# Optimization experiments

Measured on AMD Instinct MI355X. Metric: run time of the kernel, lower is better.

## Reference

```python
import jax, jax.numpy as jnp
import numpy as np

B = 32768          # batch size (positions)
PIECES = 32        # max active features per position
NNZ = B * PIECES
FT_OUT = 512
NFEAT = 768        # 64 squares * 6 piece types * 2 colors


def setup_inputs() -> dict:
    key = jax.random.key(0)
    k1, k2, k3, k4, k5, k6 = jax.random.split(key, 6)
    rows = jnp.repeat(jnp.arange(B, dtype=jnp.int64), PIECES)  # batch index per nnz
    stm_cols = jax.random.randint(k1, (NNZ,), 0, NFEAT, dtype=jnp.int64)
    nstm_cols = jax.random.randint(k2, (NNZ,), 0, NFEAT, dtype=jnp.int64)
    stm_indices = jnp.stack([rows, stm_cols], axis=0)   # [2, NNZ]
    nstm_indices = jnp.stack([rows, nstm_cols], axis=0)  # [2, NNZ]
    values = jnp.ones((NNZ,), dtype=jnp.float32)
    ft_w = jax.random.normal(k3, (FT_OUT, NFEAT), dtype=jnp.float32) * 0.05
    ft_b = jax.random.normal(k4, (FT_OUT,), dtype=jnp.float32) * 0.05
    out_w = jax.random.normal(k5, (1, 2 * FT_OUT), dtype=jnp.float32) * 0.05
    out_b = jax.random.normal(k6, (1,), dtype=jnp.float32) * 0.05
    return {
        "stm_indices": stm_indices,
        "nstm_indices": nstm_indices,
        "values": values,
        "size": B,
        "ft_w": ft_w,
        "ft_b": ft_b,
        "out_w": out_w,
        "out_b": out_b,
    }


def reference(stm_indices, nstm_indices, values, size, ft_w, ft_b, out_w, out_b):
    # sparse_coo_tensor(...).to_dense(): scatter-add values into dense [size, 768]
    board_stm = jnp.zeros((size, NFEAT), dtype=values.dtype).at[
        stm_indices[0], stm_indices[1]].add(values)
    board_nstm = jnp.zeros((size, NFEAT), dtype=values.dtype).at[
        nstm_indices[0], nstm_indices[1]].add(values)
    # shared feature transformer Linear(768, ft_out)
    stm_ft = board_stm @ ft_w.T + ft_b    # [B, FT_OUT]
    nstm_ft = board_nstm @ ft_w.T + ft_b  # [B, FT_OUT]
    hidden = jnp.clip(jnp.concatenate([stm_ft, nstm_ft], axis=1), 0.0, 1.0)
    return jax.nn.sigmoid(hidden @ out_w.T + out_b)  # [B, 1]
```

## Files before the change

kernel.cpp:

```cpp
#include <hip/hip_runtime.h>

#define BATCH  32768
#define PIECES 32
#define NNZ    (BATCH * PIECES)
#define FT_OUT 512
#define NFEAT  768
#define WSCALE 400.0f

#define POS_PER_BLOCK 32
#define NTHREADS 512
#define NBLOCKS (BATCH / POS_PER_BLOCK)
#define ROW_PITCH 784
#define SIDE_BYTES (POS_PER_BLOCK * ROW_PITCH)
#define PACC_OFF (2 * SIDE_BYTES)
#define LDS_TOTAL (PACC_OFF + 128)

typedef int v4i  __attribute__((ext_vector_type(4)));
typedef int v16i __attribute__((ext_vector_type(16)));

__global__ __launch_bounds__(256) void pack_w_i8(
    const float* __restrict__ ft_w, unsigned char* __restrict__ bpk)
{
    int gid = blockIdx.x * 256 + threadIdx.x;
    int t   = gid / 1536;
    int rem = gid - t * 1536;
    int s   = rem >> 6;
    int l   = rem & 63;
    int g   = l >> 5, ln = l & 31;
    int n   = t * 32 + ln;
    const float* src = ft_w + n * NFEAT + s * 32 + g * 16;
    unsigned ud[4];
    #pragma unroll
    for (int d = 0; d < 4; ++d) {
        unsigned u = 0;
        #pragma unroll
        for (int b = 0; b < 4; ++b) {
            float q = rintf(src[4 * d + b] * WSCALE);
            q = fminf(fmaxf(q, -127.0f), 127.0f);
            u |= ((unsigned)(int)q & 0xffu) << (8 * b);
        }
        ud[d] = u;
    }
    *(uint4*)(bpk + gid * 16) = make_uint4(ud[0], ud[1], ud[2], ud[3]);
}

__global__ __launch_bounds__(NTHREADS, 4) void nn_mfma(
    const int*   __restrict__ stm_idx,
    const int*   __restrict__ nstm_idx,
    const float* __restrict__ values,
    const unsigned char* __restrict__ bpk,
    const float* __restrict__ ft_b,
    const float* __restrict__ out_w,
    const float* __restrict__ out_b,
    float*       __restrict__ out)
{
    extern __shared__ __align__(16) unsigned char lds[];
    unsigned* ldsw = (unsigned*)lds;
    float*    pacc = (float*)(lds + PACC_OFF);

    const int tid  = threadIdx.x;
    const int pos0 = blockIdx.x * POS_PER_BLOCK;

    for (int i = tid; i < LDS_TOTAL / 16; i += NTHREADS)
        ((uint4*)lds)[i] = make_uint4(0u, 0u, 0u, 0u);
    __syncthreads();

    #pragma unroll
    for (int it = 0; it < 4; ++it) {
        int i    = tid + it * NTHREADS;
        int side = i >> 10;
        int r    = i & 1023;
        int pos  = r >> 5;
        int nnz  = pos0 * PIECES + r;
        int col  = side ? nstm_idx[NNZ + nnz] : stm_idx[NNZ + nnz];
        int vq   = (int)rintf(values[nnz]);
        int dw   = (side * SIDE_BYTES + pos * ROW_PITCH) >> 2;
        atomicAdd(&ldsw[dw + (col >> 2)], (unsigned)vq << (8 * (col & 3)));
    }
    __syncthreads();

    const int lane = tid & 63, wv = tid >> 6;
    const int ln = lane & 31, g = lane >> 5;
    const float inv_s = 1.0f / WSCALE;

    v16i acc[2][2];
    #pragma unroll
    for (int q = 0; q < 2; ++q)
        #pragma unroll
        for (int sd = 0; sd < 2; ++sd)
            #pragma unroll
            for (int e = 0; e < 16; ++e) acc[q][sd][e] = 0;

    const unsigned char* a0p = lds + ln * ROW_PITCH + g * 16;
    const unsigned char* a1p = a0p + SIDE_BYTES;
    const unsigned char* bp0 = bpk + ((wv * 2 + 0) * 24) * 1024 + lane * 16;
    const unsigned char* bp1 = bpk + ((wv * 2 + 1) * 24) * 1024 + lane * 16;

    #pragma unroll 4
    for (int ks = 0; ks < 24; ++ks) {
        uint4 aw0 = *(const uint4*)(a0p + ks * 32);
        uint4 aw1 = *(const uint4*)(a1p + ks * 32);
        uint4 bw0 = *(const uint4*)(bp0 + ks * 1024);
        uint4 bw1 = *(const uint4*)(bp1 + ks * 1024);
        v4i af0 = __builtin_bit_cast(v4i, aw0);
        v4i af1 = __builtin_bit_cast(v4i, aw1);
        v4i bf0 = __builtin_bit_cast(v4i, bw0);
        v4i bf1 = __builtin_bit_cast(v4i, bw1);
        acc[0][0] = __builtin_amdgcn_mfma_i32_32x32x32_i8(af0, bf0, acc[0][0], 0, 0, 0);
        acc[0][1] = __builtin_amdgcn_mfma_i32_32x32x32_i8(af1, bf0, acc[0][1], 0, 0, 0);
        acc[1][0] = __builtin_amdgcn_mfma_i32_32x32x32_i8(af0, bf1, acc[1][0], 0, 0, 0);
        acc[1][1] = __builtin_amdgcn_mfma_i32_32x32x32_i8(af1, bf1, acc[1][1], 0, 0, 0);
    }

    float pp[16];
    #pragma unroll
    for (int r = 0; r < 16; ++r) pp[r] = 0.f;

    #pragma unroll
    for (int q = 0; q < 2; ++q) {
        int   n    = (wv * 2 + q) * 32 + ln;
        float bias = ft_b[n];
        float ow0  = out_w[n];
        float ow1  = out_w[FT_OUT + n];
        #pragma unroll
        for (int r = 0; r < 16; ++r) {
            float h0 = fminf(fmaxf((float)acc[q][0][r] * inv_s + bias, 0.f), 1.f);
            float h1 = fminf(fmaxf((float)acc[q][1][r] * inv_s + bias, 0.f), 1.f);
            pp[r] += h0 * ow0 + h1 * ow1;
        }
    }

    #pragma unroll
    for (int r = 0; r < 16; ++r) {
        float v = pp[r];
        v += __shfl_xor(v, 16, 64);
        v += __shfl_xor(v,  8, 64);
        v += __shfl_xor(v,  4, 64);
        v += __shfl_xor(v,  2, 64);
        v += __shfl_xor(v,  1, 64);
        if (ln == 0) {
            int m = (r & 3) + 8 * (r >> 2) + 4 * g;
            atomicAdd(&pacc[m], v);
        }
    }
    __syncthreads();

    if (tid < POS_PER_BLOCK) {
        float p = pacc[tid] + out_b[0];
        out[pos0 + tid] = 1.0f / (1.0f + expf(-p));
    }
}

extern "C" void kernel_launch(void* const* d_in, const int* in_sizes, int n_in,
                              void* d_out, int out_size, void* d_ws, size_t ws_size,
                              hipStream_t stream)
{
    const int*   stm    = (const int*)  d_in[0];
    const int*   nstm   = (const int*)  d_in[1];
    const float* values = (const float*)d_in[2];
    const float* ft_w   = (const float*)d_in[4];
    const float* ft_b   = (const float*)d_in[5];
    const float* out_w  = (const float*)d_in[6];
    const float* out_b  = (const float*)d_in[7];

    unsigned char* bpk = (unsigned char*)d_ws;

    (void)hipFuncSetAttribute((const void*)nn_mfma,
                              hipFuncAttributeMaxDynamicSharedMemorySize,
                              LDS_TOTAL);

    pack_w_i8<<<dim3(96), dim3(256), 0, stream>>>(ft_w, bpk);
    nn_mfma<<<dim3(NBLOCKS), dim3(NTHREADS), LDS_TOTAL, stream>>>(
        stm, nstm, values, bpk, ft_b, out_w, out_b, (float*)d_out);
}
```

Baseline: 108.5 us.

## Prefetch sparse indices before LDS clear and software-pipeline MFMA operand loads

Global loads of feature columns and values are now issued before the LDS zeroing and barrier, so their latency overlaps the clear. The MFMA k-loop is fully unrolled and double-buffered, loading the next step's LDS and global operands while the current MFMAs run. Together these aim to hide memory latency in a latency-bound per-block kernel. The cost is extra registers from the full unroll and the held operands, which could reduce occupancy at the 4-block launch bound.

```diff
diff --git a/kernel.cpp b/kernel.cpp
--- a/kernel.cpp
+++ b/kernel.cpp
@@ -61,6 +61,17 @@
     const int tid  = threadIdx.x;
     const int pos0 = blockIdx.x * POS_PER_BLOCK;
 
+    int colv[4], vqv[4];
+    #pragma unroll
+    for (int it = 0; it < 4; ++it) {
+        int i    = tid + it * NTHREADS;
+        int side = i >> 10;
+        int r    = i & 1023;
+        int nnz  = pos0 * PIECES + r;
+        colv[it] = side ? nstm_idx[NNZ + nnz] : stm_idx[NNZ + nnz];
+        vqv[it]  = (int)rintf(values[nnz]);
+    }
+
     for (int i = tid; i < LDS_TOTAL / 16; i += NTHREADS)
         ((uint4*)lds)[i] = make_uint4(0u, 0u, 0u, 0u);
     __syncthreads();
@@ -69,13 +80,10 @@
     for (int it = 0; it < 4; ++it) {
         int i    = tid + it * NTHREADS;
         int side = i >> 10;
-        int r    = i & 1023;
-        int pos  = r >> 5;
-        int nnz  = pos0 * PIECES + r;
-        int col  = side ? nstm_idx[NNZ + nnz] : stm_idx[NNZ + nnz];
-        int vq   = (int)rintf(values[nnz]);
+        int pos  = (i & 1023) >> 5;
         int dw   = (side * SIDE_BYTES + pos * ROW_PITCH) >> 2;
-        atomicAdd(&ldsw[dw + (col >> 2)], (unsigned)vq << (8 * (col & 3)));
+        atomicAdd(&ldsw[dw + (colv[it] >> 2)],
+                  (unsigned)vqv[it] << (8 * (colv[it] & 3)));
     }
     __syncthreads();
 
@@ -96,12 +104,19 @@
     const unsigned char* bp0 = bpk + ((wv * 2 + 0) * 24) * 1024 + lane * 16;
     const unsigned char* bp1 = bpk + ((wv * 2 + 1) * 24) * 1024 + lane * 16;
 
-    #pragma unroll 4
+    uint4 aw0 = *(const uint4*)(a0p);
+    uint4 aw1 = *(const uint4*)(a1p);
+    uint4 bw0 = *(const uint4*)(bp0);
+    uint4 bw1 = *(const uint4*)(bp1);
+    #pragma unroll
     for (int ks = 0; ks < 24; ++ks) {
-        uint4 aw0 = *(const uint4*)(a0p + ks * 32);
-        uint4 aw1 = *(const uint4*)(a1p + ks * 32);
-        uint4 bw0 = *(const uint4*)(bp0 + ks * 1024);
-        uint4 bw1 = *(const uint4*)(bp1 + ks * 1024);
+        uint4 na0, na1, nb0, nb1;
+        if (ks < 23) {
+            na0 = *(const uint4*)(a0p + (ks + 1) * 32);
+            na1 = *(const uint4*)(a1p + (ks + 1) * 32);
+            nb0 = *(const uint4*)(bp0 + (ks + 1) * 1024);
+            nb1 = *(const uint4*)(bp1 + (ks + 1) * 1024);
+        }
         v4i af0 = __builtin_bit_cast(v4i, aw0);
         v4i af1 = __builtin_bit_cast(v4i, aw1);
         v4i bf0 = __builtin_bit_cast(v4i, bw0);
@@ -110,6 +125,7 @@
         acc[0][1] = __builtin_amdgcn_mfma_i32_32x32x32_i8(af1, bf0, acc[0][1], 0, 0, 0);
         acc[1][0] = __builtin_amdgcn_mfma_i32_32x32x32_i8(af0, bf1, acc[1][0], 0, 0, 0);
         acc[1][1] = __builtin_amdgcn_mfma_i32_32x32x32_i8(af1, bf1, acc[1][1], 0, 0, 0);
+        aw0 = na0; aw1 = na1; bw0 = nb0; bw1 = nb1;
     }
 
     float pp[16];
```

Result: no change. 107.3 us (-1.0%).

## Double threads per block, one N-tile per wave, prefetch indices before LDS zero

Applied to the files above, without the earlier changes.

Doubles block size to 1024 threads so each of 16 waves computes a single 32-column output tile, halving the per-wave accumulator count and the B-fragment loads. The sparse index and value loads are issued before the LDS zeroing barrier so global latency overlaps the clear. This raises the waves available to hide the global B-weight loads, but each wave now gets less ILP (2 MFMAs per step instead of 4) and the final per-block reduction involves more waves doing LDS atomics.

```diff
diff --git a/kernel.cpp b/kernel.cpp
--- a/kernel.cpp
+++ b/kernel.cpp
@@ -8,7 +8,7 @@
 #define WSCALE 400.0f
 
 #define POS_PER_BLOCK 32
-#define NTHREADS 512
+#define NTHREADS 1024
 #define NBLOCKS (BATCH / POS_PER_BLOCK)
 #define ROW_PITCH 784
 #define SIDE_BYTES (POS_PER_BLOCK * ROW_PITCH)
@@ -44,7 +44,7 @@
     *(uint4*)(bpk + gid * 16) = make_uint4(ud[0], ud[1], ud[2], ud[3]);
 }
 
-__global__ __launch_bounds__(NTHREADS, 4) void nn_mfma(
+__global__ __launch_bounds__(NTHREADS, 8) void nn_mfma(
     const int*   __restrict__ stm_idx,
     const int*   __restrict__ nstm_idx,
     const float* __restrict__ values,
@@ -61,21 +61,29 @@
     const int tid  = threadIdx.x;
     const int pos0 = blockIdx.x * POS_PER_BLOCK;
 
+    int colv[2], vqv[2];
+    #pragma unroll
+    for (int it = 0; it < 2; ++it) {
+        int i    = tid + it * NTHREADS;
+        int side = i >> 10;
+        int r    = i & 1023;
+        int nnz  = pos0 * PIECES + r;
+        colv[it] = side ? nstm_idx[NNZ + nnz] : stm_idx[NNZ + nnz];
+        vqv[it]  = (int)rintf(values[nnz]);
+    }
+
     for (int i = tid; i < LDS_TOTAL / 16; i += NTHREADS)
         ((uint4*)lds)[i] = make_uint4(0u, 0u, 0u, 0u);
     __syncthreads();
 
     #pragma unroll
-    for (int it = 0; it < 4; ++it) {
+    for (int it = 0; it < 2; ++it) {
         int i    = tid + it * NTHREADS;
         int side = i >> 10;
-        int r    = i & 1023;
-        int pos  = r >> 5;
-        int nnz  = pos0 * PIECES + r;
-        int col  = side ? nstm_idx[NNZ + nnz] : stm_idx[NNZ + nnz];
-        int vq   = (int)rintf(values[nnz]);
+        int pos  = (i & 1023) >> 5;
         int dw   = (side * SIDE_BYTES + pos * ROW_PITCH) >> 2;
-        atomicAdd(&ldsw[dw + (col >> 2)], (unsigned)vq << (8 * (col & 3)));
+        atomicAdd(&ldsw[dw + (colv[it] >> 2)],
+                  (unsigned)vqv[it] << (8 * (colv[it] & 3)));
     }
     __syncthreads();
 
@@ -83,51 +91,36 @@
     const int ln = lane & 31, g = lane >> 5;
     const float inv_s = 1.0f / WSCALE;
 
-    v16i acc[2][2];
+    v16i acc0, acc1;
     #pragma unroll
-    for (int q = 0; q < 2; ++q)
-        #pragma unroll
-        for (int sd = 0; sd < 2; ++sd)
-            #pragma unroll
-            for (int e = 0; e < 16; ++e) acc[q][sd][e] = 0;
+    for (int e = 0; e < 16; ++e) { acc0[e] = 0; acc1[e] = 0; }
 
     const unsigned char* a0p = lds + ln * ROW_PITCH + g * 16;
     const unsigned char* a1p = a0p + SIDE_BYTES;
-    const unsigned char* bp0 = bpk + ((wv * 2 + 0) * 24) * 1024 + lane * 16;
-    const unsigned char* bp1 = bpk + ((wv * 2 + 1) * 24) * 1024 + lane * 16;
+    const unsigned char* bp  = bpk + (wv * 24) * 1024 + lane * 16;
 
     #pragma unroll 4
     for (int ks = 0; ks < 24; ++ks) {
+        uint4 bw  = *(const uint4*)(bp + ks * 1024);
         uint4 aw0 = *(const uint4*)(a0p + ks * 32);
         uint4 aw1 = *(const uint4*)(a1p + ks * 32);
-        uint4 bw0 = *(const uint4*)(bp0 + ks * 1024);
-        uint4 bw1 = *(const uint4*)(bp1 + ks * 1024);
+        v4i bf  = __builtin_bit_cast(v4i, bw);
         v4i af0 = __builtin_bit_cast(v4i, aw0);
         v4i af1 = __builtin_bit_cast(v4i, aw1);
-        v4i bf0 = __builtin_bit_cast(v4i, bw0);
-        v4i bf1 = __builtin_bit_cast(v4i, bw1);
-        acc[0][0] = __builtin_amdgcn_mfma_i32_32x32x32_i8(af0, bf0, acc[0][0], 0, 0, 0);
-        acc[0][1] = __builtin_amdgcn_mfma_i32_32x32x32_i8(af1, bf0, acc[0][1], 0, 0, 0);
-        acc[1][0] = __builtin_amdgcn_mfma_i32_32x32x32_i8(af0, bf1, acc[1][0], 0, 0, 0);
-        acc[1][1] = __builtin_amdgcn_mfma_i32_32x32x32_i8(af1, bf1, acc[1][1], 0, 0, 0);
+        acc0 = __builtin_amdgcn_mfma_i32_32x32x32_i8(af0, bf, acc0, 0, 0, 0);
+        acc1 = __builtin_amdgcn_mfma_i32_32x32x32_i8(af1, bf, acc1, 0, 0, 0);
     }
 
+    const int   n    = wv * 32 + ln;
+    const float bias = ft_b[n];
+    const float ow0  = out_w[n];
+    const float ow1  = out_w[FT_OUT + n];
     float pp[16];
     #pragma unroll
-    for (int r = 0; r < 16; ++r) pp[r] = 0.f;
-
-    #pragma unroll
-    for (int q = 0; q < 2; ++q) {
-        int   n    = (wv * 2 + q) * 32 + ln;
-        float bias = ft_b[n];
-        float ow0  = out_w[n];
-        float ow1  = out_w[FT_OUT + n];
-        #pragma unroll
-        for (int r = 0; r < 16; ++r) {
-            float h0 = fminf(fmaxf((float)acc[q][0][r] * inv_s + bias, 0.f), 1.f);
-            float h1 = fminf(fmaxf((float)acc[q][1][r] * inv_s + bias, 0.f), 1.f);
-            pp[r] += h0 * ow0 + h1 * ow1;
-        }
+    for (int r = 0; r < 16; ++r) {
+        float h0 = fminf(fmaxf((float)acc0[r] * inv_s + bias, 0.f), 1.f);
+        float h1 = fminf(fmaxf((float)acc1[r] * inv_s + bias, 0.f), 1.f);
+        pp[r] = h0 * ow0 + h1 * ow1;
     }
 
     #pragma unroll
```

After: 110.5 us. Within noise of the previous version (+1.8%).
